# Kernel optimization log

Hardware: AMD Instinct MI355X
Metric: run time of the kernel (lower is better)

Reference implementation:

```python
import jax, jax.numpy as jnp
import numpy as np

B, S, D_EMBED, D_MODEL, NUM_HEADS = 2, 2048, 1024, 1024, 16
D_K = D_MODEL // NUM_HEADS
NEG = -1e9  # stands in for torch's -sys.maxsize-1 additive mask (fp32-safe)


def setup_inputs() -> dict:
    key = jax.random.key(0)
    ks = jax.random.split(key, 12)
    s = 0.02
    return {
        "query": jax.random.normal(ks[0], (B, S, D_EMBED), jnp.float32),
        "input_embeds": jax.random.normal(ks[1], (B, S, D_EMBED), jnp.float32),
        "mask": jnp.ones((B, S), jnp.float32),
        "wq_w": jax.random.normal(ks[2], (D_MODEL, D_EMBED), jnp.float32) * s,
        "wq_b": jax.random.normal(ks[3], (D_MODEL,), jnp.float32) * s,
        "wk_w": jax.random.normal(ks[4], (D_MODEL, D_EMBED), jnp.float32) * s,
        "wk_b": jax.random.normal(ks[5], (D_MODEL,), jnp.float32) * s,
        "wv_w": jax.random.normal(ks[6], (D_MODEL, D_EMBED), jnp.float32) * s,
        "wv_b": jax.random.normal(ks[7], (D_MODEL,), jnp.float32) * s,
        "wo_w": jax.random.normal(ks[8], (D_EMBED, D_MODEL), jnp.float32) * s,
        "wo_b": jax.random.normal(ks[9], (D_EMBED,), jnp.float32) * s,
    }


def _split_heads(x):
    b, s, _ = x.shape
    return x.reshape(b, s, NUM_HEADS, D_K).transpose(0, 2, 1, 3)  # [B,H,S,d_k]


def reference(query, input_embeds, mask, wq_w, wq_b, wk_w, wk_b, wv_w, wv_b, wo_w, wo_b):
    Q = _split_heads(query @ wq_w.T + wq_b)
    K = _split_heads(input_embeds @ wk_w.T + wk_b)
    V = _split_heads(input_embeds @ wv_w.T + wv_b)
    # NOTE: original module has no 1/sqrt(d_k) scaling
    scores = jnp.einsum("bhqd,bhkd->bhqk", Q, K)
    scores = scores + (1.0 - mask)[:, None, None, :] * NEG
    attn = jax.nn.softmax(scores, axis=-1)  # [B,H,Sq,Skv]
    blended = jnp.einsum("bhqk,bhkd->bhqd", attn, V)
    b, h, sq, dk = blended.shape
    concat = blended.transpose(0, 2, 1, 3).reshape(b, sq, D_MODEL)
    out = concat @ wo_w.T + wo_b
    return out, attn
```

## Files before the change

### kernel.cpp

```cpp
#include <hip/hip_runtime.h>

#define BB 2
#define SS 2048
#define DE 1024
#define DM 1024
#define NH 16
#define DK 64
#define MM (BB*SS)

typedef _Float16 HH;
typedef _Float16 half8 __attribute__((ext_vector_type(8)));
typedef float f32x4 __attribute__((ext_vector_type(4)));

template<typename AT, typename OT>
__global__ __launch_bounds__(256) void gemm_bt(const AT* __restrict__ A,
                                               const float* __restrict__ W,
                                               const float* __restrict__ bias,
                                               OT* __restrict__ O,
                                               int M, int N, int K) {
  __shared__ HH As[128][40];
  __shared__ HH Ws[128][40];

  const int tid  = threadIdx.x;
  const int lane = tid & 63;
  const int wid  = tid >> 6;
  const int wr   = wid >> 1, wc = wid & 1;
  const int brow = blockIdx.y * 128;
  const int bcol = blockIdx.x * 128;
  const int g    = lane >> 4;
  const int c    = lane & 15;

  f32x4 acc[4][4];
  #pragma unroll
  for (int i = 0; i < 4; i++)
    #pragma unroll
    for (int j = 0; j < 4; j++) acc[i][j] = (f32x4)0.0f;

  const int srow = tid >> 1;
  const int scol = (tid & 1) * 16;

  for (int k0 = 0; k0 < K; k0 += 32) {
    {
      const AT* src = A + (size_t)(brow + srow) * K + k0 + scol;
      HH tmp[16];
      if constexpr (sizeof(AT) == 4) {
        #pragma unroll
        for (int v = 0; v < 4; v++) {
          float4 f = *reinterpret_cast<const float4*>(src + v * 4);
          tmp[v*4+0] = (HH)f.x; tmp[v*4+1] = (HH)f.y;
          tmp[v*4+2] = (HH)f.z; tmp[v*4+3] = (HH)f.w;
        }
      } else {
        #pragma unroll
        for (int v = 0; v < 2; v++) {
          half8 hv = *reinterpret_cast<const half8*>(src + v * 8);
          #pragma unroll
          for (int e = 0; e < 8; e++) tmp[v*8+e] = hv[e];
        }
      }
      *reinterpret_cast<half8*>(&As[srow][scol])     = *reinterpret_cast<half8*>(&tmp[0]);
      *reinterpret_cast<half8*>(&As[srow][scol + 8]) = *reinterpret_cast<half8*>(&tmp[8]);
    }
    {
      const float* src = W + (size_t)(bcol + srow) * K + k0 + scol;
      HH tmp[16];
      #pragma unroll
      for (int v = 0; v < 4; v++) {
        float4 f = *reinterpret_cast<const float4*>(src + v * 4);
        tmp[v*4+0] = (HH)f.x; tmp[v*4+1] = (HH)f.y;
        tmp[v*4+2] = (HH)f.z; tmp[v*4+3] = (HH)f.w;
      }
      *reinterpret_cast<half8*>(&Ws[srow][scol])     = *reinterpret_cast<half8*>(&tmp[0]);
      *reinterpret_cast<half8*>(&Ws[srow][scol + 8]) = *reinterpret_cast<half8*>(&tmp[8]);
    }
    __syncthreads();

    half8 af[4], bf[4];
    #pragma unroll
    for (int i = 0; i < 4; i++)
      af[i] = *reinterpret_cast<half8*>(&As[wr*64 + i*16 + c][g * 8]);
    #pragma unroll
    for (int j = 0; j < 4; j++)
      bf[j] = *reinterpret_cast<half8*>(&Ws[wc*64 + j*16 + c][g * 8]);
    #pragma unroll
    for (int i = 0; i < 4; i++)
      #pragma unroll
      for (int j = 0; j < 4; j++)
        acc[i][j] = __builtin_amdgcn_mfma_f32_16x16x32_f16(af[i], bf[j], acc[i][j], 0, 0, 0);
    __syncthreads();
  }

  #pragma unroll
  for (int i = 0; i < 4; i++) {
    #pragma unroll
    for (int j = 0; j < 4; j++) {
      const int col = bcol + wc*64 + j*16 + c;
      const float bv = bias[col];
      #pragma unroll
      for (int r = 0; r < 4; r++) {
        const int row = brow + wr*64 + i*16 + g*4 + r;
        O[(size_t)row * N + col] = (OT)(acc[i][j][r] + bv);
      }
    }
  }
}

__global__ __launch_bounds__(256) void attn_fused(
    const HH* __restrict__ Q, const HH* __restrict__ Kh, const HH* __restrict__ Vh,
    const float* __restrict__ mask, float* __restrict__ attn, HH* __restrict__ concat) {
  __shared__ HH Qs[64][72];
  __shared__ HH Ks[64][72];
  __shared__ HH Vt[64][72];
  __shared__ HH Ps[64][72];

  const int tid  = threadIdx.x;
  const int lane = tid & 63;
  const int w    = tid >> 6;
  const int bh   = blockIdx.y;
  const int b    = bh >> 4;
  const int h    = bh & 15;
  const int q0   = blockIdx.x * 64;
  const int g    = lane >> 4;
  const int c    = lane & 15;

  const int srow = tid >> 2;
  const int sc0  = (tid & 3) * 16;

  {
    const HH* src = Q + (size_t)(b * SS + q0 + srow) * DM + h * DK + sc0;
    *reinterpret_cast<half8*>(&Qs[srow][sc0])     = *reinterpret_cast<const half8*>(src);
    *reinterpret_cast<half8*>(&Qs[srow][sc0 + 8]) = *reinterpret_cast<const half8*>(src + 8);
  }
  __syncthreads();

  half8 aq0 = *reinterpret_cast<half8*>(&Qs[w*16 + c][g * 8]);
  half8 aq1 = *reinterpret_cast<half8*>(&Qs[w*16 + c][32 + g * 8]);

  float m[4], l[4];
  #pragma unroll
  for (int r = 0; r < 4; r++) { m[r] = -3.0e38f; l[r] = 0.0f; }

  for (int kt = 0; kt < SS / 64; kt++) {
    {
      const HH* src = Kh + (size_t)(b * SS + kt * 64 + srow) * DM + h * DK + sc0;
      *reinterpret_cast<half8*>(&Ks[srow][sc0])     = *reinterpret_cast<const half8*>(src);
      *reinterpret_cast<half8*>(&Ks[srow][sc0 + 8]) = *reinterpret_cast<const half8*>(src + 8);
    }
    __syncthreads();

    f32x4 s[4];
    #pragma unroll
    for (int f = 0; f < 4; f++) {
      half8 bk0 = *reinterpret_cast<half8*>(&Ks[f*16 + c][g * 8]);
      half8 bk1 = *reinterpret_cast<half8*>(&Ks[f*16 + c][32 + g * 8]);
      f32x4 t = (f32x4)0.0f;
      t = __builtin_amdgcn_mfma_f32_16x16x32_f16(aq0, bk0, t, 0, 0, 0);
      t = __builtin_amdgcn_mfma_f32_16x16x32_f16(aq1, bk1, t, 0, 0, 0);
      const float mv = mask[(size_t)b * SS + kt * 64 + f * 16 + c];
      const float madd = (1.0f - mv) * -1e9f;
      #pragma unroll
      for (int r = 0; r < 4; r++) t[r] += madd;
      s[f] = t;
    }
    #pragma unroll
    for (int r = 0; r < 4; r++) {
      float tm = fmaxf(fmaxf(s[0][r], s[1][r]), fmaxf(s[2][r], s[3][r]));
      for (int off = 1; off < 16; off <<= 1) tm = fmaxf(tm, __shfl_xor(tm, off));
      const float mn = fmaxf(m[r], tm);
      float rs = 0.0f;
      #pragma unroll
      for (int f = 0; f < 4; f++) rs += __expf(s[f][r] - mn);
      for (int off = 1; off < 16; off <<= 1) rs += __shfl_xor(rs, off);
      l[r] = l[r] * __expf(m[r] - mn) + rs;
      m[r] = mn;
    }
    __syncthreads();
  }

  float invl[4];
  #pragma unroll
  for (int r = 0; r < 4; r++) invl[r] = 1.0f / l[r];

  f32x4 pv[4];
  #pragma unroll
  for (int f = 0; f < 4; f++) pv[f] = (f32x4)0.0f;

  for (int kt = 0; kt < SS / 64; kt++) {
    {
      const HH* src = Kh + (size_t)(b * SS + kt * 64 + srow) * DM + h * DK + sc0;
      *reinterpret_cast<half8*>(&Ks[srow][sc0])     = *reinterpret_cast<const half8*>(src);
      *reinterpret_cast<half8*>(&Ks[srow][sc0 + 8]) = *reinterpret_cast<const half8*>(src + 8);
      const HH* vsrc = Vh + (size_t)(b * SS + kt * 64 + srow) * DM + h * DK + sc0;
      half8 v0 = *reinterpret_cast<const half8*>(vsrc);
      half8 v1 = *reinterpret_cast<const half8*>(vsrc + 8);
      #pragma unroll
      for (int e = 0; e < 8; e++) Vt[sc0 + e][srow] = v0[e];
      #pragma unroll
      for (int e = 0; e < 8; e++) Vt[sc0 + 8 + e][srow] = v1[e];
    }
    __syncthreads();

    #pragma unroll
    for (int f = 0; f < 4; f++) {
      half8 bk0 = *reinterpret_cast<half8*>(&Ks[f*16 + c][g * 8]);
      half8 bk1 = *reinterpret_cast<half8*>(&Ks[f*16 + c][32 + g * 8]);
      f32x4 t = (f32x4)0.0f;
      t = __builtin_amdgcn_mfma_f32_16x16x32_f16(aq0, bk0, t, 0, 0, 0);
      t = __builtin_amdgcn_mfma_f32_16x16x32_f16(aq1, bk1, t, 0, 0, 0);
      const float mv = mask[(size_t)b * SS + kt * 64 + f * 16 + c];
      const float madd = (1.0f - mv) * -1e9f;
      #pragma unroll
      for (int r = 0; r < 4; r++) {
        const float p = __expf(t[r] + madd - m[r]) * invl[r];
        const int qrow = w * 16 + g * 4 + r;
        attn[((size_t)bh * SS + (q0 + qrow)) * SS + kt * 64 + f * 16 + c] = p;
        Ps[qrow][f * 16 + c] = (HH)p;
      }
    }
    __syncthreads();

    half8 ap0 = *reinterpret_cast<half8*>(&Ps[w*16 + c][g * 8]);
    half8 ap1 = *reinterpret_cast<half8*>(&Ps[w*16 + c][32 + g * 8]);
    #pragma unroll
    for (int f = 0; f < 4; f++) {
      half8 bv0 = *reinterpret_cast<half8*>(&Vt[f*16 + c][g * 8]);
      half8 bv1 = *reinterpret_cast<half8*>(&Vt[f*16 + c][32 + g * 8]);
      pv[f] = __builtin_amdgcn_mfma_f32_16x16x32_f16(ap0, bv0, pv[f], 0, 0, 0);
      pv[f] = __builtin_amdgcn_mfma_f32_16x16x32_f16(ap1, bv1, pv[f], 0, 0, 0);
    }
    __syncthreads();
  }

  #pragma unroll
  for (int f = 0; f < 4; f++) {
    #pragma unroll
    for (int r = 0; r < 4; r++) {
      const int qrow = w * 16 + g * 4 + r;
      concat[(size_t)(b * SS + q0 + qrow) * DM + h * DK + f * 16 + c] = (HH)pv[f][r];
    }
  }
}

extern "C" void kernel_launch(void* const* d_in, const int* in_sizes, int n_in,
                              void* d_out, int out_size, void* d_ws, size_t ws_size,
                              hipStream_t stream) {
  const float* query = (const float*)d_in[0];
  const float* embeds = (const float*)d_in[1];
  const float* mask  = (const float*)d_in[2];
  const float* wq_w = (const float*)d_in[3];
  const float* wq_b = (const float*)d_in[4];
  const float* wk_w = (const float*)d_in[5];
  const float* wk_b = (const float*)d_in[6];
  const float* wv_w = (const float*)d_in[7];
  const float* wv_b = (const float*)d_in[8];
  const float* wo_w = (const float*)d_in[9];
  const float* wo_b = (const float*)d_in[10];

  float* out  = (float*)d_out;
  float* attn = out + (size_t)MM * DE;

  HH* Qw = (HH*)d_ws;
  HH* Kw = Qw + (size_t)MM * DM;
  HH* Vw = Kw + (size_t)MM * DM;
  HH* Cc = Vw + (size_t)MM * DM;

  dim3 gg(DM / 128, MM / 128);
  gemm_bt<float, HH><<<gg, 256, 0, stream>>>(query,  wq_w, wq_b, Qw, MM, DM, DE);
  gemm_bt<float, HH><<<gg, 256, 0, stream>>>(embeds, wk_w, wk_b, Kw, MM, DM, DE);
  gemm_bt<float, HH><<<gg, 256, 0, stream>>>(embeds, wv_w, wv_b, Vw, MM, DM, DE);

  dim3 ga(SS / 64, BB * NH);
  attn_fused<<<ga, 256, 0, stream>>>(Qw, Kw, Vw, mask, attn, Cc);

  gemm_bt<HH, float><<<gg, 256, 0, stream>>>(Cc, wo_w, wo_b, out, MM, DE, DM);
}
```

Before: 900.3 us.

## Pre-convert inputs to fp16, use direct global-to-LDS loads, batch QKV GEMMs

A new conversion kernel casts the activations and all four weight matrices to fp16 once, so the GEMMs no longer convert fp32 to fp16 in registers on every tile load. The GEMM tile loads now use global_load_lds to write straight into unpadded shared memory. The three QKV projections run as a single launch using grid z, and the attention probability writes use nontemporal stores. The extra conversion pass and workspace traffic may offset the gains, and dropping the shared-memory padding risks bank conflicts on the fragment reads.

```diff
diff --git a/kernel.cpp b/kernel.cpp
--- a/kernel.cpp
+++ b/kernel.cpp
@@ -9,17 +9,44 @@
 #define MM (BB*SS)
 
 typedef _Float16 HH;
+typedef _Float16 half4 __attribute__((ext_vector_type(4)));
 typedef _Float16 half8 __attribute__((ext_vector_type(8)));
 typedef float f32x4 __attribute__((ext_vector_type(4)));
 
-template<typename AT, typename OT>
-__global__ __launch_bounds__(256) void gemm_bt(const AT* __restrict__ A,
-                                               const float* __restrict__ W,
-                                               const float* __restrict__ bias,
-                                               OT* __restrict__ O,
-                                               int M, int N, int K) {
-  __shared__ HH As[128][40];
-  __shared__ HH Ws[128][40];
+__device__ __forceinline__ void gload_lds16(const void* g, void* l) {
+  __builtin_amdgcn_global_load_lds(
+      (const __attribute__((address_space(1))) uint32_t*)g,
+      (__attribute__((address_space(3))) uint32_t*)l, 16, 0, 0);
+}
+
+__global__ __launch_bounds__(256) void cvt6(
+    const float* __restrict__ q,  const float* __restrict__ e,
+    const float* __restrict__ wq, const float* __restrict__ wk,
+    const float* __restrict__ wv, const float* __restrict__ wo,
+    HH* qh, HH* eh, HH* wqh, HH* wkh, HH* wvh, HH* woh) {
+  const float* s; HH* d; int n4;
+  switch (blockIdx.y) {
+    case 0:  s = q;  d = qh;  n4 = MM * DE / 4; break;
+    case 1:  s = e;  d = eh;  n4 = MM * DE / 4; break;
+    case 2:  s = wq; d = wqh; n4 = DM * DE / 4; break;
+    case 3:  s = wk; d = wkh; n4 = DM * DE / 4; break;
+    case 4:  s = wv; d = wvh; n4 = DM * DE / 4; break;
+    default: s = wo; d = woh; n4 = DM * DE / 4; break;
+  }
+  for (int i = blockIdx.x * 256 + threadIdx.x; i < n4; i += gridDim.x * 256) {
+    float4 f = reinterpret_cast<const float4*>(s)[i];
+    half4 h; h[0] = (HH)f.x; h[1] = (HH)f.y; h[2] = (HH)f.z; h[3] = (HH)f.w;
+    *reinterpret_cast<half4*>(&d[(size_t)i * 4]) = h;
+  }
+}
+
+template<typename OT>
+__device__ __forceinline__ void gemm_body(const HH* __restrict__ A,
+                                          const HH* __restrict__ W,
+                                          const float* __restrict__ bias,
+                                          OT* __restrict__ O) {
+  __shared__ alignas(16) HH As[128][32];
+  __shared__ alignas(16) HH Ws[128][32];
 
   const int tid  = threadIdx.x;
   const int lane = tid & 63;
@@ -30,58 +57,29 @@
   const int g    = lane >> 4;
   const int c    = lane & 15;
 
-  f32x4 acc[4][4];
-  #pragma unroll
-  for (int i = 0; i < 4; i++)
-    #pragma unroll
-    for (int j = 0; j < 4; j++) acc[i][j] = (f32x4)0.0f;
-
-  const int srow = tid >> 1;
-  const int scol = (tid & 1) * 16;
-
-  for (int k0 = 0; k0 < K; k0 += 32) {
-    {
-      const AT* src = A + (size_t)(brow + srow) * K + k0 + scol;
-      HH tmp[16];
-      if constexpr (sizeof(AT) == 4) {
-        #pragma unroll
-        for (int v = 0; v < 4; v++) {
-          float4 f = *reinterpret_cast<const float4*>(src + v * 4);
-          tmp[v*4+0] = (HH)f.x; tmp[v*4+1] = (HH)f.y;
-          tmp[v*4+2] = (HH)f.z; tmp[v*4+3] = (HH)f.w;
-        }
-      } else {
-        #pragma unroll
-        for (int v = 0; v < 2; v++) {
-          half8 hv = *reinterpret_cast<const half8*>(src + v * 8);
-          #pragma unroll
-          for (int e = 0; e < 8; e++) tmp[v*8+e] = hv[e];
-        }
-      }
-      *reinterpret_cast<half8*>(&As[srow][scol])     = *reinterpret_cast<half8*>(&tmp[0]);
-      *reinterpret_cast<half8*>(&As[srow][scol + 8]) = *reinterpret_cast<half8*>(&tmp[8]);
-    }
-    {
-      const float* src = W + (size_t)(bcol + srow) * K + k0 + scol;
-      HH tmp[16];
-      #pragma unroll
-      for (int v = 0; v < 4; v++) {
-        float4 f = *reinterpret_cast<const float4*>(src + v * 4);
-        tmp[v*4+0] = (HH)f.x; tmp[v*4+1] = (HH)f.y;
-        tmp[v*4+2] = (HH)f.z; tmp[v*4+3] = (HH)f.w;
-      }
-      *reinterpret_cast<half8*>(&Ws[srow][scol])     = *reinterpret_cast<half8*>(&tmp[0]);
-      *reinterpret_cast<half8*>(&Ws[srow][scol + 8]) = *reinterpret_cast<half8*>(&tmp[8]);
-    }
+  f32x4 acc[4][4] = {};
+
+  const int lr = tid >> 2;
+  const int lc = (tid & 3) * 8;
+  const HH* a0 = A + (size_t)(brow + lr) * 1024 + lc;
+  const HH* w0 = W + (size_t)(bcol + lr) * 1024 + lc;
+  char* ldsA = (char*)As + tid * 16;
+  char* ldsW = (char*)Ws + tid * 16;
+
+  for (int k0 = 0; k0 < 1024; k0 += 32) {
+    gload_lds16(a0 + k0,             ldsA);
+    gload_lds16(a0 + 64 * 1024 + k0, ldsA + 4096);
+    gload_lds16(w0 + k0,             ldsW);
+    gload_lds16(w0 + 64 * 1024 + k0, ldsW + 4096);
     __syncthreads();
 
     half8 af[4], bf[4];
     #pragma unroll
     for (int i = 0; i < 4; i++)
-      af[i] = *reinterpret_cast<half8*>(&As[wr*64 + i*16 + c][g * 8]);
+      af[i] = *reinterpret_cast<half8*>(&As[wr * 64 + i * 16 + c][g * 8]);
     #pragma unroll
     for (int j = 0; j < 4; j++)
-      bf[j] = *reinterpret_cast<half8*>(&Ws[wc*64 + j*16 + c][g * 8]);
+      bf[j] = *reinterpret_cast<half8*>(&Ws[wc * 64 + j * 16 + c][g * 8]);
     #pragma unroll
     for (int i = 0; i < 4; i++)
       #pragma unroll
@@ -94,15 +92,35 @@
   for (int i = 0; i < 4; i++) {
     #pragma unroll
     for (int j = 0; j < 4; j++) {
-      const int col = bcol + wc*64 + j*16 + c;
+      const int col = bcol + wc * 64 + j * 16 + c;
       const float bv = bias[col];
       #pragma unroll
       for (int r = 0; r < 4; r++) {
-        const int row = brow + wr*64 + i*16 + g*4 + r;
-        O[(size_t)row * N + col] = (OT)(acc[i][j][r] + bv);
+        const int row = brow + wr * 64 + i * 16 + g * 4 + r;
+        O[(size_t)row * 1024 + col] = (OT)(acc[i][j][r] + bv);
       }
     }
   }
+}
+
+__global__ __launch_bounds__(256) void gemm_qkv(
+    const HH* __restrict__ Aq, const HH* __restrict__ Ae,
+    const HH* __restrict__ Wq, const HH* __restrict__ Wk, const HH* __restrict__ Wv,
+    const float* __restrict__ bq, const float* __restrict__ bk, const float* __restrict__ bv,
+    HH* Oq, HH* Ok, HH* Ov) {
+  const HH* A; const HH* W; const float* bias; HH* O;
+  switch (blockIdx.z) {
+    case 0:  A = Aq; W = Wq; bias = bq; O = Oq; break;
+    case 1:  A = Ae; W = Wk; bias = bk; O = Ok; break;
+    default: A = Ae; W = Wv; bias = bv; O = Ov; break;
+  }
+  gemm_body<HH>(A, W, bias, O);
+}
+
+__global__ __launch_bounds__(256) void gemm_o(
+    const HH* __restrict__ A, const HH* __restrict__ W,
+    const float* __restrict__ bias, float* __restrict__ O) {
+  gemm_body<float>(A, W, bias, O);
 }
 
 __global__ __launch_bounds__(256) void attn_fused(
@@ -133,8 +151,8 @@
   }
   __syncthreads();
 
-  half8 aq0 = *reinterpret_cast<half8*>(&Qs[w*16 + c][g * 8]);
-  half8 aq1 = *reinterpret_cast<half8*>(&Qs[w*16 + c][32 + g * 8]);
+  half8 aq0 = *reinterpret_cast<half8*>(&Qs[w * 16 + c][g * 8]);
+  half8 aq1 = *reinterpret_cast<half8*>(&Qs[w * 16 + c][32 + g * 8]);
 
   float m[4], l[4];
   #pragma unroll
@@ -151,8 +169,8 @@
     f32x4 s[4];
     #pragma unroll
     for (int f = 0; f < 4; f++) {
-      half8 bk0 = *reinterpret_cast<half8*>(&Ks[f*16 + c][g * 8]);
-      half8 bk1 = *reinterpret_cast<half8*>(&Ks[f*16 + c][32 + g * 8]);
+      half8 bk0 = *reinterpret_cast<half8*>(&Ks[f * 16 + c][g * 8]);
+      half8 bk1 = *reinterpret_cast<half8*>(&Ks[f * 16 + c][32 + g * 8]);
       f32x4 t = (f32x4)0.0f;
       t = __builtin_amdgcn_mfma_f32_16x16x32_f16(aq0, bk0, t, 0, 0, 0);
       t = __builtin_amdgcn_mfma_f32_16x16x32_f16(aq1, bk1, t, 0, 0, 0);
@@ -202,8 +220,8 @@
 
     #pragma unroll
     for (int f = 0; f < 4; f++) {
-      half8 bk0 = *reinterpret_cast<half8*>(&Ks[f*16 + c][g * 8]);
-      half8 bk1 = *reinterpret_cast<half8*>(&Ks[f*16 + c][32 + g * 8]);
+      half8 bk0 = *reinterpret_cast<half8*>(&Ks[f * 16 + c][g * 8]);
+      half8 bk1 = *reinterpret_cast<half8*>(&Ks[f * 16 + c][32 + g * 8]);
       f32x4 t = (f32x4)0.0f;
       t = __builtin_amdgcn_mfma_f32_16x16x32_f16(aq0, bk0, t, 0, 0, 0);
       t = __builtin_amdgcn_mfma_f32_16x16x32_f16(aq1, bk1, t, 0, 0, 0);
@@ -213,18 +231,19 @@
       for (int r = 0; r < 4; r++) {
         const float p = __expf(t[r] + madd - m[r]) * invl[r];
         const int qrow = w * 16 + g * 4 + r;
-        attn[((size_t)bh * SS + (q0 + qrow)) * SS + kt * 64 + f * 16 + c] = p;
+        __builtin_nontemporal_store(
+            p, &attn[((size_t)bh * SS + (q0 + qrow)) * SS + kt * 64 + f * 16 + c]);
         Ps[qrow][f * 16 + c] = (HH)p;
       }
     }
     __syncthreads();
 
-    half8 ap0 = *reinterpret_cast<half8*>(&Ps[w*16 + c][g * 8]);
-    half8 ap1 = *reinterpret_cast<half8*>(&Ps[w*16 + c][32 + g * 8]);
+    half8 ap0 = *reinterpret_cast<half8*>(&Ps[w * 16 + c][g * 8]);
+    half8 ap1 = *reinterpret_cast<half8*>(&Ps[w * 16 + c][32 + g * 8]);
     #pragma unroll
     for (int f = 0; f < 4; f++) {
-      half8 bv0 = *reinterpret_cast<half8*>(&Vt[f*16 + c][g * 8]);
-      half8 bv1 = *reinterpret_cast<half8*>(&Vt[f*16 + c][32 + g * 8]);
+      half8 bv0 = *reinterpret_cast<half8*>(&Vt[f * 16 + c][g * 8]);
+      half8 bv1 = *reinterpret_cast<half8*>(&Vt[f * 16 + c][32 + g * 8]);
       pv[f] = __builtin_amdgcn_mfma_f32_16x16x32_f16(ap0, bv0, pv[f], 0, 0, 0);
       pv[f] = __builtin_amdgcn_mfma_f32_16x16x32_f16(ap1, bv1, pv[f], 0, 0, 0);
     }
@@ -244,9 +263,9 @@
 extern "C" void kernel_launch(void* const* d_in, const int* in_sizes, int n_in,
                               void* d_out, int out_size, void* d_ws, size_t ws_size,
                               hipStream_t stream) {
-  const float* query = (const float*)d_in[0];
+  const float* query  = (const float*)d_in[0];
   const float* embeds = (const float*)d_in[1];
-  const float* mask  = (const float*)d_in[2];
+  const float* mask   = (const float*)d_in[2];
   const float* wq_w = (const float*)d_in[3];
   const float* wq_b = (const float*)d_in[4];
   const float* wk_w = (const float*)d_in[5];
@@ -259,18 +278,24 @@
   float* out  = (float*)d_out;
   float* attn = out + (size_t)MM * DE;
 
-  HH* Qw = (HH*)d_ws;
-  HH* Kw = Qw + (size_t)MM * DM;
-  HH* Vw = Kw + (size_t)MM * DM;
-  HH* Cc = Vw + (size_t)MM * DM;
-
-  dim3 gg(DM / 128, MM / 128);
-  gemm_bt<float, HH><<<gg, 256, 0, stream>>>(query,  wq_w, wq_b, Qw, MM, DM, DE);
-  gemm_bt<float, HH><<<gg, 256, 0, stream>>>(embeds, wk_w, wk_b, Kw, MM, DM, DE);
-  gemm_bt<float, HH><<<gg, 256, 0, stream>>>(embeds, wv_w, wv_b, Vw, MM, DM, DE);
-
-  dim3 ga(SS / 64, BB * NH);
-  attn_fused<<<ga, 256, 0, stream>>>(Qw, Kw, Vw, mask, attn, Cc);
-
-  gemm_bt<HH, float><<<gg, 256, 0, stream>>>(Cc, wo_w, wo_b, out, MM, DE, DM);
-}
+  HH* Qh  = (HH*)d_ws;
+  HH* Eh  = Qh  + (size_t)MM * DE;
+  HH* Wqh = Eh  + (size_t)MM * DE;
+  HH* Wkh = Wqh + (size_t)DM * DE;
+  HH* Wvh = Wkh + (size_t)DM * DE;
+  HH* Woh = Wvh + (size_t)DM * DE;
+  HH* Qw  = Woh + (size_t)DM * DE;
+  HH* Kw  = Qw  + (size_t)MM * DM;
+  HH* Vw  = Kw  + (size_t)MM * DM;
+  HH* Cc  = Vw  + (size_t)MM * DM;
+
+  cvt6<<<dim3(1024, 6), 256, 0, stream>>>(query, embeds, wq_w, wk_w, wv_w, wo_w,
+                                          Qh, Eh, Wqh, Wkh, Wvh, Woh);
+
+  gemm_qkv<<<dim3(8, 32, 3), 256, 0, stream>>>(Qh, Eh, Wqh, Wkh, Wvh,
+                                               wq_b, wk_b, wv_b, Qw, Kw, Vw);
+
+  attn_fused<<<dim3(SS / 64, BB * NH), 256, 0, stream>>>(Qw, Kw, Vw, mask, attn, Cc);
+
+  gemm_o<<<dim3(8, 32), 256, 0, stream>>>(Cc, Woh, wo_b, out);
+}
```

Result: faster. 785.4 us (-12.8%).
